# Performance work log

Measured on AMD Instinct MI355X. Metric: run time of the kernel, lower is better.

Reference implementation:

```python
import jax, jax.numpy as jnp
import numpy as np

# Model config (matches init_kwargs)
B, N, D = 4, 4096, 1024
H, DH = 16, 64            # heads, dim_head (H*DH == D)
SEG, RATIO = 64, 2        # LongNet segment length and dilation ratio
DFF = 4 * D
EPS = 1e-5


def layer_norm(x, g, b):
    m = jnp.mean(x, axis=-1, keepdims=True)
    v = jnp.var(x, axis=-1, keepdims=True)
    return (x - m) * jax.lax.rsqrt(v + EPS) * g + b


def dilated_attention(x, wq, bq, wk, bk, wv, bv, wo, bo):
    # LongNet-style dilated attention: split into segments of SEG tokens,
    # each head attends over every RATIO-th token of its segment, with the
    # dilation offset distributed across heads (offset = head % RATIO).
    b, n, d = x.shape
    G = n // SEG          # number of segments
    M = SEG // RATIO      # dilated segment length
    scale = DH ** -0.5

    def proj_split(w, bias):
        t = (x @ w + bias).reshape(b, G, SEG, H, DH)
        return t.transpose(0, 1, 3, 2, 4)  # [B, G, H, SEG, DH]

    q = proj_split(wq, bq)
    k = proj_split(wk, bk)
    v = proj_split(wv, bv)

    # per-head dilated indices within a segment: [H, M]
    idx = (jnp.arange(H)[:, None] % RATIO) + RATIO * jnp.arange(M)[None, :]
    gidx = idx[None, None, :, :, None]  # broadcast to [1,1,H,M,1]
    qs = jnp.take_along_axis(q, gidx, axis=3)  # [B,G,H,M,DH]
    ks = jnp.take_along_axis(k, gidx, axis=3)
    vs = jnp.take_along_axis(v, gidx, axis=3)

    scores = jnp.einsum('bghmd,bghnd->bghmn', qs, ks) * scale
    p = jax.nn.softmax(scores, axis=-1)
    o = jnp.einsum('bghmn,bghnd->bghmd', p, vs)  # [B,G,H,M,DH]

    # scatter dilated outputs back to full segment positions (zeros elsewhere)
    full = jnp.zeros((b, G, H, SEG, DH), dtype=o.dtype)
    full = full.at[:, :, jnp.arange(H)[:, None], idx, :].set(o)
    out = full.transpose(0, 1, 3, 2, 4).reshape(b, n, d)
    return out @ wo + bo


def setup_inputs() -> dict:
    key = jax.random.key(0)
    ks = jax.random.split(key, 8)
    sd = D ** -0.5
    inp = {
        'x': jax.random.normal(ks[0], (B, N, D), jnp.float32),
        'gamma': jnp.ones((D,), jnp.float32),  # shared pre-norm (beta is zero buffer)
        'wq': jax.random.normal(ks[1], (D, D), jnp.float32) * sd,
        'bq': jnp.zeros((D,), jnp.float32),
        'wk': jax.random.normal(ks[2], (D, D), jnp.float32) * sd,
        'bk': jnp.zeros((D,), jnp.float32),
        'wv': jax.random.normal(ks[3], (D, D), jnp.float32) * sd,
        'bv': jnp.zeros((D,), jnp.float32),
        'wo': jax.random.normal(ks[4], (D, D), jnp.float32) * sd,
        'bo': jnp.zeros((D,), jnp.float32),
        'ff_g': jnp.ones((D,), jnp.float32),   # FFN LayerNorm weight
        'ff_b': jnp.zeros((D,), jnp.float32),  # FFN LayerNorm bias
        'w1': jax.random.normal(ks[5], (D, DFF), jnp.float32) * sd,
        'b1': jnp.zeros((DFF,), jnp.float32),
        'w2': jax.random.normal(ks[6], (DFF, D), jnp.float32) * (DFF ** -0.5),
        'b2': jnp.zeros((D,), jnp.float32),
    }
    return inp


def reference(x, gamma, wq, bq, wk, bk, wv, bv, wo, bo, ff_g, ff_b, w1, b1, w2, b2):
    zero = jnp.zeros((D,), x.dtype)
    # attention sub-block (pre-norm, residual)
    h = layer_norm(x, gamma, zero)
    attn = dilated_attention(h, wq, bq, wk, bk, wv, bv, wo, bo)
    x = x + attn
    # FFN sub-block (outer shared norm, then FFN's own LayerNorm per FeedForward)
    h = layer_norm(x, gamma, zero)
    h = layer_norm(h, ff_g, ff_b)
    h = jax.nn.gelu(h @ w1 + b1, approximate=False) @ w2 + b2
    return x + h
```

## Files before the change

kernel.cpp:

```cpp
#include <hip/hip_runtime.h>
#include <hip/hip_bf16.h>
#include <math.h>

#define NTOK 16384
#define DM   1024
#define NQKV 3072
#define DFF  4096

typedef __bf16 bf16;
typedef __bf16 bf16x8 __attribute__((ext_vector_type(8)));
typedef float  f32x4  __attribute__((ext_vector_type(4)));

__device__ __forceinline__ void gload_lds16(const bf16* g, bf16* l) {
  __builtin_amdgcn_global_load_lds((const __attribute__((address_space(1))) void*)g,
                                   (__attribute__((address_space(3))) void*)l,
                                   16, 0, 0);
}

__global__ __launch_bounds__(256)
void transpose_cvt(const float* __restrict__ src, bf16* __restrict__ dst, int K, int N)
{
  __shared__ float t[32][33];
  const int tx = threadIdx.x & 31, ty = threadIdx.x >> 5;
  const int n0 = blockIdx.x * 32, k0 = blockIdx.y * 32;
#pragma unroll
  for (int i = 0; i < 4; ++i)
    t[ty + 8*i][tx] = src[(size_t)(k0 + ty + 8*i) * N + n0 + tx];
  __syncthreads();
#pragma unroll
  for (int i = 0; i < 4; ++i)
    dst[(size_t)(n0 + ty + 8*i) * K + k0 + tx] = (bf16)t[tx][ty + 8*i];
}

__global__ void concat_bias(const float* __restrict__ bq, const float* __restrict__ bk,
                            const float* __restrict__ bv, float* __restrict__ o)
{
  int i = blockIdx.x * 256 + threadIdx.x;
  o[i] = (i < 1024) ? bq[i] : (i < 2048 ? bk[i - 1024] : bv[i - 2048]);
}

__global__ __launch_bounds__(256)
void ln1_kernel(const float* __restrict__ x, const float* __restrict__ gamma,
                bf16* __restrict__ out)
{
  __shared__ float2 red[4];
  const int row = blockIdx.x, tid = threadIdx.x;
  const float4 v = ((const float4*)(x + (size_t)row * DM))[tid];
  float s  = v.x + v.y + v.z + v.w;
  float s2 = v.x*v.x + v.y*v.y + v.z*v.z + v.w*v.w;
#pragma unroll
  for (int m = 32; m >= 1; m >>= 1) { s += __shfl_xor(s, m); s2 += __shfl_xor(s2, m); }
  if ((tid & 63) == 0) red[tid >> 6] = make_float2(s, s2);
  __syncthreads();
  float S  = red[0].x + red[1].x + red[2].x + red[3].x;
  float S2 = red[0].y + red[1].y + red[2].y + red[3].y;
  const float mean = S * (1.0f / DM);
  const float var  = S2 * (1.0f / DM) - mean * mean;
  const float rs   = rsqrtf(var + 1e-5f);
  const float4 g = ((const float4*)gamma)[tid];
  union { bf16 b[4]; uint2 u; } o;
  o.b[0] = (bf16)((v.x - mean) * rs * g.x);
  o.b[1] = (bf16)((v.y - mean) * rs * g.y);
  o.b[2] = (bf16)((v.z - mean) * rs * g.z);
  o.b[3] = (bf16)((v.w - mean) * rs * g.w);
  *(uint2*)(out + (size_t)row * DM + tid * 4) = o.u;
}

__global__ __launch_bounds__(256)
void ln2_kernel(const float* __restrict__ x, const float* __restrict__ gamma,
                const float* __restrict__ ffg, const float* __restrict__ ffb,
                bf16* __restrict__ out)
{
  __shared__ float2 red[4];
  const int row = blockIdx.x, tid = threadIdx.x;
  const float4 v = ((const float4*)(x + (size_t)row * DM))[tid];
  float s  = v.x + v.y + v.z + v.w;
  float s2 = v.x*v.x + v.y*v.y + v.z*v.z + v.w*v.w;
#pragma unroll
  for (int m = 32; m >= 1; m >>= 1) { s += __shfl_xor(s, m); s2 += __shfl_xor(s2, m); }
  if ((tid & 63) == 0) red[tid >> 6] = make_float2(s, s2);
  __syncthreads();
  float S  = red[0].x + red[1].x + red[2].x + red[3].x;
  float S2 = red[0].y + red[1].y + red[2].y + red[3].y;
  float mean = S * (1.0f / DM);
  float var  = S2 * (1.0f / DM) - mean * mean;
  float rs   = rsqrtf(var + 1e-5f);
  const float4 g = ((const float4*)ffg)[tid];
  const float4 gg = ((const float4*)gamma)[tid];
  float y0 = (v.x - mean) * rs * gg.x;
  float y1 = (v.y - mean) * rs * gg.y;
  float y2 = (v.z - mean) * rs * gg.z;
  float y3 = (v.w - mean) * rs * gg.w;
  __syncthreads();
  s  = y0 + y1 + y2 + y3;
  s2 = y0*y0 + y1*y1 + y2*y2 + y3*y3;
#pragma unroll
  for (int m = 32; m >= 1; m >>= 1) { s += __shfl_xor(s, m); s2 += __shfl_xor(s2, m); }
  if ((tid & 63) == 0) red[tid >> 6] = make_float2(s, s2);
  __syncthreads();
  S  = red[0].x + red[1].x + red[2].x + red[3].x;
  S2 = red[0].y + red[1].y + red[2].y + red[3].y;
  mean = S * (1.0f / DM);
  var  = S2 * (1.0f / DM) - mean * mean;
  rs   = rsqrtf(var + 1e-5f);
  const float4 bb = ((const float4*)ffb)[tid];
  union { bf16 b[4]; uint2 u; } o;
  o.b[0] = (bf16)((y0 - mean) * rs * g.x + bb.x);
  o.b[1] = (bf16)((y1 - mean) * rs * g.y + bb.y);
  o.b[2] = (bf16)((y2 - mean) * rs * g.z + bb.z);
  o.b[3] = (bf16)((y3 - mean) * rs * g.w + bb.w);
  *(uint2*)(out + (size_t)row * DM + tid * 4) = o.u;
}


template<int EPI>
__global__ __launch_bounds__(256, 4)
void gemm128(const bf16* __restrict__ A, int lda,
             const bf16* __restrict__ Bt,
             const float* __restrict__ bias,
             const float* res, int ldres,
             void* Cout, int ldc, int K, int nblk)
{
  __shared__ __align__(16) bf16 lds[16384];
  const int tid = threadIdx.x, lane = tid & 63, wave = tid >> 6;
  const int wm = wave >> 1, wn = wave & 1;
  const int l16 = lane & 15, lg = lane >> 4;

  int id = blockIdx.x;
  id = (id & 7) * (nblk >> 3) + (id >> 3);
  const int row0 = (id & 127) << 7;
  const int col0 = (id >> 7) << 7;
  const int NT = K >> 6;

  const char* Ab = (const char*)A;
  const char* Bb = (const char*)Bt;
  unsigned oA[4], oB[4];
  {
    const int lr = tid >> 3;
    const int lc = tid & 7;
#pragma unroll
    for (int it = 0; it < 4; ++it) {
      const int r = it * 32 + lr;
      const int gc = ((lc ^ (r & 7)) << 3);
      oA[it] = (unsigned)(((row0 + r) * lda + gc) * 2);
      oB[it] = (unsigned)(((col0 + r) * K   + gc) * 2);
    }
  }

#define STAGE() do { \
    gload_lds16((const bf16*)(Ab + oA[0]), lds        + tid * 8); \
    gload_lds16((const bf16*)(Ab + oA[1]), lds + 2048 + tid * 8); \
    gload_lds16((const bf16*)(Ab + oA[2]), lds + 4096 + tid * 8); \
    gload_lds16((const bf16*)(Ab + oA[3]), lds + 6144 + tid * 8); \
    gload_lds16((const bf16*)(Bb + oB[0]), lds + 8192 + tid * 8); \
    gload_lds16((const bf16*)(Bb + oB[1]), lds + 10240 + tid * 8); \
    gload_lds16((const bf16*)(Bb + oB[2]), lds + 12288 + tid * 8); \
    gload_lds16((const bf16*)(Bb + oB[3]), lds + 14336 + tid * 8); \
    oA[0] += 128; oA[1] += 128; oA[2] += 128; oA[3] += 128; \
    oB[0] += 128; oB[1] += 128; oB[2] += 128; oB[3] += 128; } while (0)

  int aoff[4][2], boff[4][2];
#pragma unroll
  for (int i = 0; i < 4; ++i) {
    const int ra = wm * 64 + i * 16 + l16;
    const int rb = wn * 64 + i * 16 + l16;
#pragma unroll
    for (int kk = 0; kk < 2; ++kk) {
      aoff[i][kk] = ra * 64 + (((kk * 4 + lg) ^ (ra & 7)) << 3);
      boff[i][kk] = 8192 + rb * 64 + (((kk * 4 + lg) ^ (rb & 7)) << 3);
    }
  }

  f32x4 acc[4][4] = {};

  STAGE();
  for (int t = 0; t < NT; ++t) {
    __syncthreads();
    bf16x8 af[4][2];
#pragma unroll
    for (int i = 0; i < 4; ++i) {
      af[i][0] = *(const bf16x8*)&lds[aoff[i][0]];
      af[i][1] = *(const bf16x8*)&lds[aoff[i][1]];
    }
#pragma unroll
    for (int j = 0; j < 4; ++j) {
      bf16x8 b0 = *(const bf16x8*)&lds[boff[j][0]];
      bf16x8 b1 = *(const bf16x8*)&lds[boff[j][1]];
#pragma unroll
      for (int i = 0; i < 4; ++i) {
        acc[i][j] = __builtin_amdgcn_mfma_f32_16x16x32_bf16(af[i][0], b0, acc[i][j], 0, 0, 0);
        acc[i][j] = __builtin_amdgcn_mfma_f32_16x16x32_bf16(af[i][1], b1, acc[i][j], 0, 0, 0);
      }
    }
    __syncthreads();
    if (t + 1 < NT) STAGE();
  }

#pragma unroll
  for (int i = 0; i < 4; ++i) {
    const int m0 = row0 + wm * 64 + i * 16 + lg * 4;
#pragma unroll
    for (int j = 0; j < 4; ++j) {
      const int n = col0 + wn * 64 + j * 16 + l16;
      const float bv = bias[n];
#pragma unroll
      for (int r = 0; r < 4; ++r) {
        const long m = m0 + r;
        float v = acc[i][j][r] + bv;
        if constexpr (EPI == 0) {
          ((bf16*)Cout)[m * ldc + n] = (bf16)v;
        } else if constexpr (EPI == 1) {
          ((float*)Cout)[m * ldc + n] = v + res[m * ldres + n];
        } else {
          float gl = 0.5f * v * (1.0f + erff(v * 0.70710678118654752f));
          ((bf16*)Cout)[m * ldc + n] = (bf16)gl;
        }
      }
    }
  }
}

__global__ __launch_bounds__(64)
void attn_kernel(bf16* qkv)
{
  __shared__ bf16 Plds[32 * 32];
  __shared__ bf16 vT[64 * 32];
  const int blk = blockIdx.x;
  const int h = blk & 15;
  const int g = (blk >> 4) & 63;
  const int b = blk >> 10;
  const int par = h & 1;
  const int lane = threadIdx.x;
  const int l16 = lane & 15, lg = lane >> 4;
  const long base = ((long)b * 4096 + g * 64) * NQKV;

  bf16x8 qf[2][2], kf[2][2];
#pragma unroll
  for (int mb = 0; mb < 2; ++mb) {
    const int s = par + 2 * (mb * 16 + l16);
    const bf16* qrow = qkv + base + (long)s * NQKV + h * 64;
#pragma unroll
    for (int kk = 0; kk < 2; ++kk) {
      qf[mb][kk] = *(const bf16x8*)(qrow + kk * 32 + lg * 8);
      kf[mb][kk] = *(const bf16x8*)(qrow + 1024 + kk * 32 + lg * 8);
    }
  }

#pragma unroll
  for (int it = 0; it < 4; ++it) {
    const int kr  = it * 8 + (lane >> 3);
    const int dh0 = (lane & 7) * 8;
    const int s = par + 2 * kr;
    union { uint4 u; bf16 e[8]; } vv;
    vv.u = *(const uint4*)(qkv + base + (long)s * NQKV + 2048 + h * 64 + dh0);
#pragma unroll
    for (int j = 0; j < 8; ++j)
      vT[(dh0 + j) * 32 + kr] = vv.e[j];
  }

  f32x4 sc[2][2] = {};
#pragma unroll
  for (int mb = 0; mb < 2; ++mb)
#pragma unroll
    for (int nb = 0; nb < 2; ++nb)
#pragma unroll
      for (int kk = 0; kk < 2; ++kk)
        sc[mb][nb] = __builtin_amdgcn_mfma_f32_16x16x32_bf16(qf[mb][kk], kf[nb][kk], sc[mb][nb], 0, 0, 0);

  float pr[2][2][4];
#pragma unroll
  for (int mb = 0; mb < 2; ++mb)
#pragma unroll
    for (int r = 0; r < 4; ++r) {
      float a0 = sc[mb][0][r] * 0.125f, a1 = sc[mb][1][r] * 0.125f;
      float mx = fmaxf(a0, a1);
#pragma unroll
      for (int msk = 8; msk >= 1; msk >>= 1) mx = fmaxf(mx, __shfl_xor(mx, msk));
      float e0 = expf(a0 - mx), e1 = expf(a1 - mx);
      float sm = e0 + e1;
#pragma unroll
      for (int msk = 8; msk >= 1; msk >>= 1) sm += __shfl_xor(sm, msk);
      float inv = 1.0f / sm;
      pr[mb][0][r] = e0 * inv;
      pr[mb][1][r] = e1 * inv;
    }

  __syncthreads();
#pragma unroll
  for (int mb = 0; mb < 2; ++mb)
#pragma unroll
    for (int nb = 0; nb < 2; ++nb)
#pragma unroll
      for (int r = 0; r < 4; ++r)
        Plds[(mb * 16 + lg * 4 + r) * 32 + nb * 16 + l16] = (bf16)pr[mb][nb][r];
  __syncthreads();

  bf16x8 pa[2], vb[4];
#pragma unroll
  for (int mb = 0; mb < 2; ++mb)
    pa[mb] = *(const bf16x8*)&Plds[(mb * 16 + l16) * 32 + lg * 8];
#pragma unroll
  for (int nb = 0; nb < 4; ++nb)
    vb[nb] = *(const bf16x8*)&vT[(nb * 16 + l16) * 32 + lg * 8];
  f32x4 oc[2][4] = {};
#pragma unroll
  for (int mb = 0; mb < 2; ++mb)
#pragma unroll
    for (int nb = 0; nb < 4; ++nb)
      oc[mb][nb] = __builtin_amdgcn_mfma_f32_16x16x32_bf16(pa[mb], vb[nb], oc[mb][nb], 0, 0, 0);

#pragma unroll
  for (int mb = 0; mb < 2; ++mb)
#pragma unroll
    for (int nb = 0; nb < 4; ++nb)
#pragma unroll
      for (int r = 0; r < 4; ++r) {
        const int m = mb * 16 + lg * 4 + r;
        const int s = par + 2 * m;
        qkv[base + (long)s * NQKV + h * 64 + nb * 16 + l16] = (bf16)oc[mb][nb][r];
      }
  const uint4 z = make_uint4(0, 0, 0, 0);
#pragma unroll
  for (int it = 0; it < 4; ++it) {
    const int r2 = it * 8 + (lane >> 3);
    const int s = (1 - par) + 2 * r2;
    *(uint4*)(qkv + base + (long)s * NQKV + h * 64 + (lane & 7) * 8) = z;
  }
}

extern "C" void kernel_launch(void* const* d_in, const int* in_sizes, int n_in,
                              void* d_out, int out_size, void* d_ws, size_t ws_size,
                              hipStream_t stream)
{
  const float* x     = (const float*)d_in[0];
  const float* gamma = (const float*)d_in[1];
  const float* wq = (const float*)d_in[2];  const float* bq = (const float*)d_in[3];
  const float* wk = (const float*)d_in[4];  const float* bk = (const float*)d_in[5];
  const float* wv = (const float*)d_in[6];  const float* bv = (const float*)d_in[7];
  const float* wo = (const float*)d_in[8];  const float* bo = (const float*)d_in[9];
  const float* ffg = (const float*)d_in[10]; const float* ffb = (const float*)d_in[11];
  const float* w1 = (const float*)d_in[12]; const float* b1 = (const float*)d_in[13];
  const float* w2 = (const float*)d_in[14]; const float* b2 = (const float*)d_in[15];

  char* p = (char*)d_ws;
  bf16* Wqkv_t = (bf16*)p; p += (size_t)NQKV * DM * 2;
  bf16* Wo_t   = (bf16*)p; p += (size_t)DM * DM * 2;
  bf16* W1_t   = (bf16*)p; p += (size_t)DFF * DM * 2;
  bf16* W2_t   = (bf16*)p; p += (size_t)DM * DFF * 2;
  float* bqkv  = (float*)p; p += (size_t)NQKV * 4;
  bf16* hbuf   = (bf16*)p; p += (size_t)NTOK * DM * 2;
  bf16* qkv    = (bf16*)p; p += (size_t)NTOK * DFF * 2;
  float* xnew  = (float*)d_out;

  dim3 b256(256);
  transpose_cvt<<<dim3(32, 32),  b256, 0, stream>>>(wq, Wqkv_t,               DM, DM);
  transpose_cvt<<<dim3(32, 32),  b256, 0, stream>>>(wk, Wqkv_t + 1024 * 1024, DM, DM);
  transpose_cvt<<<dim3(32, 32),  b256, 0, stream>>>(wv, Wqkv_t + 2048 * 1024, DM, DM);
  transpose_cvt<<<dim3(32, 32),  b256, 0, stream>>>(wo, Wo_t, DM, DM);
  transpose_cvt<<<dim3(128, 32), b256, 0, stream>>>(w1, W1_t, DM, DFF);
  transpose_cvt<<<dim3(32, 128), b256, 0, stream>>>(w2, W2_t, DFF, DM);
  concat_bias<<<12, b256, 0, stream>>>(bq, bk, bv, bqkv);

  ln1_kernel<<<NTOK, b256, 0, stream>>>(x, gamma, hbuf);

  gemm128<0><<<dim3(128 * 24), b256, 0, stream>>>(
      hbuf, DM, Wqkv_t, bqkv, nullptr, 0, qkv, NQKV, DM, 128 * 24);

  attn_kernel<<<4096, dim3(64), 0, stream>>>(qkv);

  gemm128<1><<<dim3(128 * 8), b256, 0, stream>>>(
      qkv, NQKV, Wo_t, bo, x, DM, xnew, DM, DM, 128 * 8);

  ln2_kernel<<<NTOK, b256, 0, stream>>>(xnew, gamma, ffg, ffb, hbuf);

  gemm128<2><<<dim3(128 * 32), b256, 0, stream>>>(
      hbuf, DM, W1_t, b1, nullptr, 0, qkv, DFF, DM, 128 * 32);

  gemm128<1><<<dim3(128 * 8), b256, 0, stream>>>(
      qkv, DFF, W2_t, b2, xnew, DM, (float*)d_out, DM, DFF, 128 * 8);
}
```

Measured before the change: 679.6 us.

## Double-buffer LDS in bf16 GEMM to overlap global loads with MFMA

Doubles the GEMM's LDS to two 32KB stages so the next K-tile is prefetched via global_load_lds into the alternate buffer while MFMAs run on the current one. The loop is unrolled by two and uses raw s_barrier plus explicit waitcnt, with a sched_barrier between the LDS fragment loads and the MFMA block. This aims to hide global load latency and cut one barrier per iteration. In exchange, launch bounds drop from 4 to 2 blocks per CU, which lowers occupancy and the latency hiding that came from running more blocks.

```diff
diff --git a/kernel.cpp b/kernel.cpp
--- a/kernel.cpp
+++ b/kernel.cpp
@@ -16,6 +16,11 @@
                                    (__attribute__((address_space(3))) void*)l,
                                    16, 0, 0);
 }
+
+#define BAR()    asm volatile("s_barrier" ::: "memory")
+#define SB0()    __builtin_amdgcn_sched_barrier(0)
+#define LGKM0()  asm volatile("s_waitcnt lgkmcnt(0)" ::: "memory")
+#define VMW0()   asm volatile("s_waitcnt vmcnt(0)" ::: "memory")
 
 __global__ __launch_bounds__(256)
 void transpose_cvt(const float* __restrict__ src, bf16* __restrict__ dst, int K, int N)
@@ -114,14 +119,14 @@
 
 
 template<int EPI>
-__global__ __launch_bounds__(256, 4)
+__global__ __launch_bounds__(256, 2)
 void gemm128(const bf16* __restrict__ A, int lda,
              const bf16* __restrict__ Bt,
              const float* __restrict__ bias,
              const float* res, int ldres,
              void* Cout, int ldc, int K, int nblk)
 {
-  __shared__ __align__(16) bf16 lds[16384];
+  __shared__ __align__(16) bf16 lds[32768];
   const int tid = threadIdx.x, lane = tid & 63, wave = tid >> 6;
   const int wm = wave >> 1, wn = wave & 1;
   const int l16 = lane & 15, lg = lane >> 4;
@@ -147,15 +152,15 @@
     }
   }
 
-#define STAGE() do { \
-    gload_lds16((const bf16*)(Ab + oA[0]), lds        + tid * 8); \
-    gload_lds16((const bf16*)(Ab + oA[1]), lds + 2048 + tid * 8); \
-    gload_lds16((const bf16*)(Ab + oA[2]), lds + 4096 + tid * 8); \
-    gload_lds16((const bf16*)(Ab + oA[3]), lds + 6144 + tid * 8); \
-    gload_lds16((const bf16*)(Bb + oB[0]), lds + 8192 + tid * 8); \
-    gload_lds16((const bf16*)(Bb + oB[1]), lds + 10240 + tid * 8); \
-    gload_lds16((const bf16*)(Bb + oB[2]), lds + 12288 + tid * 8); \
-    gload_lds16((const bf16*)(Bb + oB[3]), lds + 14336 + tid * 8); \
+#define STAGE(BASE) do { \
+    gload_lds16((const bf16*)(Ab + oA[0]), lds + (BASE)         + tid * 8); \
+    gload_lds16((const bf16*)(Ab + oA[1]), lds + (BASE) + 2048  + tid * 8); \
+    gload_lds16((const bf16*)(Ab + oA[2]), lds + (BASE) + 4096  + tid * 8); \
+    gload_lds16((const bf16*)(Ab + oA[3]), lds + (BASE) + 6144  + tid * 8); \
+    gload_lds16((const bf16*)(Bb + oB[0]), lds + (BASE) + 8192  + tid * 8); \
+    gload_lds16((const bf16*)(Bb + oB[1]), lds + (BASE) + 10240 + tid * 8); \
+    gload_lds16((const bf16*)(Bb + oB[2]), lds + (BASE) + 12288 + tid * 8); \
+    gload_lds16((const bf16*)(Bb + oB[3]), lds + (BASE) + 14336 + tid * 8); \
     oA[0] += 128; oA[1] += 128; oA[2] += 128; oA[3] += 128; \
     oB[0] += 128; oB[1] += 128; oB[2] += 128; oB[3] += 128; } while (0)
 
@@ -173,27 +178,31 @@
 
   f32x4 acc[4][4] = {};
 
-  STAGE();
-  for (int t = 0; t < NT; ++t) {
-    __syncthreads();
-    bf16x8 af[4][2];
-#pragma unroll
-    for (int i = 0; i < 4; ++i) {
-      af[i][0] = *(const bf16x8*)&lds[aoff[i][0]];
-      af[i][1] = *(const bf16x8*)&lds[aoff[i][1]];
-    }
-#pragma unroll
-    for (int j = 0; j < 4; ++j) {
-      bf16x8 b0 = *(const bf16x8*)&lds[boff[j][0]];
-      bf16x8 b1 = *(const bf16x8*)&lds[boff[j][1]];
-#pragma unroll
-      for (int i = 0; i < 4; ++i) {
-        acc[i][j] = __builtin_amdgcn_mfma_f32_16x16x32_bf16(af[i][0], b0, acc[i][j], 0, 0, 0);
-        acc[i][j] = __builtin_amdgcn_mfma_f32_16x16x32_bf16(af[i][1], b1, acc[i][j], 0, 0, 0);
-      }
-    }
-    __syncthreads();
-    if (t + 1 < NT) STAGE();
+#define GTILE(TB, NB, STG) do { \
+    if (STG) STAGE(NB); \
+    bf16x8 af[4][2], bf[4][2]; \
+    _Pragma("unroll") \
+    for (int i = 0; i < 4; ++i) { \
+      af[i][0] = *(const bf16x8*)&lds[(TB) + aoff[i][0]]; \
+      af[i][1] = *(const bf16x8*)&lds[(TB) + aoff[i][1]]; \
+      bf[i][0] = *(const bf16x8*)&lds[(TB) + boff[i][0]]; \
+      bf[i][1] = *(const bf16x8*)&lds[(TB) + boff[i][1]]; \
+    } \
+    LGKM0(); SB0(); \
+    _Pragma("unroll") \
+    for (int j = 0; j < 4; ++j) \
+      _Pragma("unroll") \
+      for (int i = 0; i < 4; ++i) { \
+        acc[i][j] = __builtin_amdgcn_mfma_f32_16x16x32_bf16(af[i][0], bf[j][0], acc[i][j], 0, 0, 0); \
+        acc[i][j] = __builtin_amdgcn_mfma_f32_16x16x32_bf16(af[i][1], bf[j][1], acc[i][j], 0, 0, 0); \
+      } \
+    if (STG) VMW0(); \
+    BAR(); } while (0)
+
+  STAGE(0); VMW0(); BAR();
+  for (int t = 0; t < NT; t += 2) {
+    GTILE(0, 16384, true);
+    GTILE(16384, 0, (t + 2 < NT));
   }
 
 #pragma unroll
```

Measured after the change: 763.0 us. 12.3% more time.
